# Kernel optimization log

Measured on AMD Instinct MI355X. Metric: run time of the kernel, lower is better.

The kernel has to match this reference:

```python
import jax, jax.numpy as jnp
from jax import lax
import numpy as np

SCALE = 1.0   # self.scale
EPS = 1e-12
CHUNK = 512   # points processed per chunk to bound [P,T,3] temporaries


def _closest_sqdist(p, a, b, c):
    """Squared distance from points p:[P,3] to triangles (a,b,c):[T,3] -> [P,T].
    Ericson's closest-point-on-triangle, fully vectorized."""
    ab = b - a
    ac = c - a
    bc = c - b
    ap = p[:, None, :] - a[None, :, :]
    bp = p[:, None, :] - b[None, :, :]
    cp = p[:, None, :] - c[None, :, :]
    d1 = jnp.einsum('td,ptd->pt', ab, ap)
    d2 = jnp.einsum('td,ptd->pt', ac, ap)
    d3 = jnp.einsum('td,ptd->pt', ab, bp)
    d4 = jnp.einsum('td,ptd->pt', ac, bp)
    d5 = jnp.einsum('td,ptd->pt', ab, cp)
    d6 = jnp.einsum('td,ptd->pt', ac, cp)
    va = d3 * d6 - d5 * d4
    vb = d5 * d2 - d1 * d6
    vc = d1 * d4 - d3 * d2

    def sdiv(n, d):  # NaN/Inf-safe division (branch is masked out by where anyway)
        return n / jnp.where(jnp.abs(d) < EPS, 1.0, d)

    t_ab = sdiv(d1, d1 - d3)[..., None]
    t_ac = sdiv(d2, d2 - d6)[..., None]
    t_bc = sdiv(d4 - d3, (d4 - d3) + (d5 - d6))[..., None]
    denom = va + vb + vc
    v_in = sdiv(vb, denom)[..., None]
    w_in = sdiv(vc, denom)[..., None]

    # base case: interior of the face; then overwrite with edge / vertex regions
    cl = a[None] + v_in * ab[None] + w_in * ac[None]
    cl = jnp.where(((va <= 0) & (d4 - d3 >= 0) & (d5 - d6 >= 0))[..., None],
                   b[None] + t_bc * bc[None], cl)   # edge BC
    cl = jnp.where(((vb <= 0) & (d2 >= 0) & (d6 <= 0))[..., None],
                   a[None] + t_ac * ac[None], cl)   # edge AC
    cl = jnp.where(((vc <= 0) & (d1 >= 0) & (d3 <= 0))[..., None],
                   a[None] + t_ab * ab[None], cl)   # edge AB
    cl = jnp.where(((d6 >= 0) & (d5 <= d6))[..., None], c[None], cl)  # vertex C
    cl = jnp.where(((d3 >= 0) & (d4 <= d3))[..., None], b[None], cl)  # vertex B
    cl = jnp.where(((d1 <= 0) & (d2 <= 0))[..., None], a[None], cl)   # vertex A
    diff = p[:, None, :] - cl
    return jnp.sum(diff * diff, axis=-1)


def setup_inputs():
    key = jax.random.key(0)
    k1, k2, k3 = jax.random.split(key, 3)
    vertices = jax.random.normal(k1, (4, 3, 16, 16, 16), dtype=jnp.float32)
    pc = jax.random.uniform(k2, (4, 4096, 3), dtype=jnp.float32)
    faces = jax.random.randint(k3, (8192, 3), 0, 4096, dtype=jnp.int32)
    return {"vertices": vertices, "pc": pc, "faces": faces}


def reference(vertices, pc, faces):
    B = vertices.shape[0]
    v = jax.nn.sigmoid(vertices)                     # self.normalization
    pos = jnp.moveaxis(v, 1, -1).reshape(B, -1, 3)   # permute(1,2,3,0).view(-1,3)
    pts = pc * SCALE                                 # _scale_points
    # pymesh path drops all-zero points; emulate with a mask (scaling keeps zeros zero)
    mask = jnp.any(pc != 0.0, axis=-1).astype(pts.dtype)  # [B,N]

    def per_batch(args):
        posb, pb, mb = args
        a = posb[faces[:, 0]]
        b = posb[faces[:, 1]]
        c = posb[faces[:, 2]]
        n_chunks = pb.shape[0] // CHUNK

        def chunk_min(pch):  # [CHUNK,3] -> [CHUNK] nearest sq-dist over all tris
            return jnp.min(_closest_sqdist(pch, a, b, c), axis=-1)

        d = lax.map(chunk_min, pb.reshape(n_chunks, CHUNK, 3)).reshape(-1)
        cnt = jnp.maximum(jnp.sum(mb), 1.0)
        return jnp.sum(d * mb) / cnt                 # mean(squared_distances)

    losses = lax.map(per_batch, (pos, pts, mask))    # [B]
    return jnp.mean(losses)
```

## Files before the change

### kernel.cpp

```cpp
#include <hip/hip_runtime.h>
#include <math.h>
#include <float.h>

#define NB 4
#define NP 4096
#define NT 8192
#define TSE 12
#define TEE 20
#define EPSD 1e-12
#define MNS 32
#define MTCH (NT/MNS)
#define VCH 16
#define VLEN (NP/VCH)

__device__ __forceinline__ float sigm(float x) { return 1.0f / (1.0f + expf(-x)); }

__device__ __forceinline__ float tri_dist(
    float px, float py, float pz,
    float ax, float ay, float az,
    float abx, float aby, float abz,
    float acx, float acy, float acz,
    float aa, float am, float cc,
    float raa, float rcc, float rbb,
    float rden, float den, float bb, float k1)
{
  float apx = px - ax, apy = py - ay, apz = pz - az;
  float d1   = apx*abx + apy*aby + apz*abz;
  float d2   = apx*acx + apy*acy + apz*acz;
  float apap = apx*apx + apy*apy + apz*apz;
  float vb = d1*cc - d2*am;
  float vc = d2*aa - d1*am;
  float va = den - vb - vc;
  float di = apap - (vb*d1 + vc*d2)*rden;
  float t2 = d1 + d1;
  float tab = fminf(fmaxf(d1*raa, 0.0f), 1.0f);
  float dAB = apap + tab*(tab*aa - t2);
  float t4 = d2 + d2;
  float tac = fminf(fmaxf(d2*rcc, 0.0f), 1.0f);
  float dAC = apap + tac*(tac*cc - t4);
  float e   = d2 - d1 + k1;
  float tbc = fminf(fmaxf(e*rbb, 0.0f), 1.0f);
  float distB = apap - t2 + aa;
  float dBC = distB + tbc*(tbc*bb - (e + e));
  float m3 = fminf(fminf(dAB, dAC), dBC);
  bool in = (vb >= 0.0f) & (vc >= 0.0f) & (va > 0.0f);
  return in ? di : m3;
}

__global__ __launch_bounds__(256) void vert_kernel(
    const float* __restrict__ verts, float* __restrict__ pos)
{
  int i = blockIdx.x * 256 + threadIdx.x;
  if (i < NB * 3 * NP) pos[i] = sigm(verts[i]);
}

__global__ __launch_bounds__(256) void prep_kernel(
    const float* __restrict__ pos, const int* __restrict__ faces,
    float* __restrict__ triS, float* __restrict__ triE)
{
  int idx = blockIdx.x * 256 + threadIdx.x;
  if (idx >= NB * NT) return;
  int b = idx >> 13;
  int t = idx & (NT - 1);
  int f0 = faces[3*t + 0], f1 = faces[3*t + 1], f2i = faces[3*t + 2];
  const float* pb = pos + (size_t)b * 3 * NP;
  float ax = pb[f0],  ay = pb[NP + f0],  az = pb[2*NP + f0];
  float bx = pb[f1],  by = pb[NP + f1],  bz = pb[2*NP + f1];
  float cx = pb[f2i], cy = pb[NP + f2i], cz = pb[2*NP + f2i];
  float abx = bx - ax, aby = by - ay, abz = bz - az;
  float acx = cx - ax, acy = cy - ay, acz = cz - az;
  double aa = (double)abx*abx + (double)aby*aby + (double)abz*abz;
  double am = (double)abx*acx + (double)aby*acy + (double)abz*acz;
  double cc = (double)acx*acx + (double)acy*acy + (double)acz*acz;
  double den = aa*cc - am*am;
  double bb  = aa - 2.0*am + cc;
  float raa  = (fabs(aa)  < EPSD) ? 1.0f : (float)(1.0/aa);
  float rcc  = (fabs(cc)  < EPSD) ? 1.0f : (float)(1.0/cc);
  float rbb  = (fabs(bb)  < EPSD) ? 1.0f : (float)(1.0/bb);
  float rden = (fabs(den) < EPSD) ? 0.0f : (float)(1.0/den);
  double nx = (double)aby*acz - (double)abz*acy;
  double ny = (double)abz*acx - (double)abx*acz;
  double nz = (double)abx*acy - (double)aby*acx;
  double rs = (fabs(den) < EPSD) ? 0.0 : 1.0 / sqrt(den * 1.02);
  float nhx = (float)(nx * rs), nhy = (float)(ny * rs), nhz = (float)(nz * rs);
  float w = (float)(-(nx*ax + ny*ay + nz*az) * rs);
  float lox = fminf(ax, fminf(bx, cx)), hix = fmaxf(ax, fmaxf(bx, cx));
  float loy = fminf(ay, fminf(by, cy)), hiy = fmaxf(ay, fmaxf(by, cy));
  float loz = fminf(az, fminf(bz, cz)), hiz = fmaxf(az, fmaxf(bz, cz));
  float* rs_ = triS + (size_t)idx * TSE;
  rs_[0] = nhx; rs_[1] = nhy; rs_[2] = nhz; rs_[3]  = w;
  rs_[4] = lox; rs_[5] = loy; rs_[6] = loz; rs_[7]  = hix;
  rs_[8] = hiy; rs_[9] = hiz; rs_[10] = 0.0f; rs_[11] = 0.0f;
  float* re = triE + (size_t)idx * TEE;
  re[0]  = ax;  re[1]  = ay;  re[2]  = az;  re[3]  = abx;
  re[4]  = aby; re[5]  = abz; re[6]  = acx; re[7]  = acy;
  re[8]  = acz; re[9]  = (float)aa; re[10] = (float)am; re[11] = (float)cc;
  re[12] = raa; re[13] = rcc; re[14] = rbb; re[15] = rden;
  re[16] = (float)den; re[17] = (float)bb; re[18] = (float)(aa - am); re[19] = 0.0f;
}

__global__ __launch_bounds__(256) void seed_kernel(
    const float* __restrict__ pos, const float* __restrict__ pc,
    float* __restrict__ partS)
{
  int bid  = blockIdx.x;
  int pblk = bid & 15;
  int vc   = (bid >> 4) & (VCH - 1);
  int b    = bid >> 8;
  int p    = pblk * 256 + threadIdx.x;
  const float* pp = pc + ((size_t)b * NP + p) * 3;
  float px = pp[0], py = pp[1], pz = pp[2];
  const float* base = pos + (size_t)b * 3 * NP + vc * VLEN;
  const float4* X = (const float4*)(base);
  const float4* Y = (const float4*)(base + NP);
  const float4* Z = (const float4*)(base + 2 * NP);
  float m = FLT_MAX;
  #pragma unroll 4
  for (int v = 0; v < VLEN / 4; ++v) {
    float4 vx = X[v], vy = Y[v], vz = Z[v];
    {
      float dx = px - vx.x, dy = py - vy.x, dz = pz - vz.x;
      m = fminf(m, dx*dx + dy*dy + dz*dz);
    }
    {
      float dx = px - vx.y, dy = py - vy.y, dz = pz - vz.y;
      m = fminf(m, dx*dx + dy*dy + dz*dz);
    }
    {
      float dx = px - vx.z, dy = py - vy.z, dz = pz - vz.z;
      m = fminf(m, dx*dx + dy*dy + dz*dz);
    }
    {
      float dx = px - vx.w, dy = py - vy.w, dz = pz - vz.w;
      m = fminf(m, dx*dx + dy*dy + dz*dz);
    }
  }
  partS[((size_t)b * VCH + vc) * NP + p] = m;
}

__global__ __launch_bounds__(256) void main_kernel(
    const float* __restrict__ triS, const float* __restrict__ triE,
    const float* __restrict__ pc, const float* __restrict__ partS,
    float* __restrict__ partM)
{
  __shared__ unsigned qbuf[4][128];
  __shared__ unsigned wmind[4][64];

  int bid  = blockIdx.x;
  int pblk = bid & 15;
  int s    = (bid >> 4) & (MNS - 1);
  int b    = bid >> 9;
  int tid  = threadIdx.x;
  int wave = tid >> 6, lane = tid & 63;
  int p    = pblk * 256 + tid;

  const float* pp = pc + ((size_t)b * NP + p) * 3;
  float px = pp[0], py = pp[1], pz = pp[2];

  float mind = FLT_MAX;
  #pragma unroll
  for (int j = 0; j < VCH; ++j)
    mind = fminf(mind, partS[((size_t)b * VCH + j) * NP + p]);
  wmind[wave][lane] = __float_as_uint(mind);
  float mth = mind + 1e-8f;

  unsigned qcnt = 0u, qd = 0u;
  const float* triEB = triE + (size_t)b * NT * TEE;
  int tg0 = s * MTCH;
  const float4* Rs = (const float4*)(triS + (size_t)(b * NT + tg0) * TSE);

#define DRAIN_BATCH(NACT)                                                     \
  {                                                                           \
    unsigned ent = qbuf[wave][(qd + (unsigned)lane) & 127u];                  \
    if ((unsigned)lane < (unsigned)(NACT)) {                                  \
      int te  = (int)(ent >> 6);                                              \
      int src = (int)(ent & 63u);                                             \
      float qx = __shfl(px, src, 64);                                         \
      float qy = __shfl(py, src, 64);                                         \
      float qz = __shfl(pz, src, 64);                                         \
      const float* rr = triEB + (size_t)te * TEE;                             \
      float4 w1 = *(const float4*)(rr + 0);                                   \
      float4 w2 = *(const float4*)(rr + 4);                                   \
      float4 w3 = *(const float4*)(rr + 8);                                   \
      float4 w4 = *(const float4*)(rr + 12);                                  \
      float4 w5 = *(const float4*)(rr + 16);                                  \
      float dd = fmaxf(tri_dist(qx, qy, qz,                                   \
                                w1.x, w1.y, w1.z,                             \
                                w1.w, w2.x, w2.y,                             \
                                w2.z, w2.w, w3.x,                             \
                                w3.y, w3.z, w3.w,                             \
                                w4.x, w4.y, w4.z,                             \
                                w4.w, w5.x, w5.y, w5.z), 0.0f);               \
      atomicMin(&wmind[wave][src], __float_as_uint(dd));                      \
    }                                                                         \
    qd += (unsigned)(NACT);                                                   \
    mind = fminf(mind, __uint_as_float(wmind[wave][lane]));                   \
    mth  = mind + 1e-8f;                                                      \
  }

#define SCAN_ITER(Q0, Q1, Q2, TIDX)                                           \
  {                                                                           \
    float sN = fmaf(pz, (Q0).z, fmaf(py, (Q0).y, fmaf(px, (Q0).x, (Q0).w)));  \
    float dx = fmaxf(fmaxf((Q1).x - px, px - (Q1).w), 0.0f);                  \
    float dy = fmaxf(fmaxf((Q1).y - py, py - (Q2).x), 0.0f);                  \
    float dz = fmaxf(fmaxf((Q1).z - pz, pz - (Q2).y), 0.0f);                  \
    float bb2 = dx*dx + dy*dy + dz*dz;                                        \
    bool pred = (sN * sN < mth) & (bb2 * 0.98f < mth);                        \
    unsigned long long mask = __ballot(pred);                                 \
    if (mask) {                                                               \
      if (pred) {                                                             \
        int prefix = __builtin_amdgcn_mbcnt_hi((unsigned)(mask >> 32),        \
                       __builtin_amdgcn_mbcnt_lo((unsigned)mask, 0));         \
        qbuf[wave][(qcnt + (unsigned)prefix) & 127u] =                        \
            ((unsigned)(TIDX) << 6) | (unsigned)lane;                         \
      }                                                                       \
      qcnt += (unsigned)__builtin_popcountll(mask);                           \
      if (qcnt - qd >= 64u) DRAIN_BATCH(64u);                                 \
    }                                                                         \
  }

  float4 a0 = Rs[0], a1 = Rs[1], a2 = Rs[2];
  float4 b0 = Rs[3], b1 = Rs[4], b2 = Rs[5];
  int tg = tg0;
  for (int g = 0; g < MTCH / 2; ++g) {
    const float4* Rn = Rs + 6;
    float4 c0 = Rn[0], c1 = Rn[1], c2 = Rn[2];
    float4 d0 = Rn[3], d1 = Rn[4], d2 = Rn[5];
    SCAN_ITER(a0, a1, a2, tg + 0);
    SCAN_ITER(b0, b1, b2, tg + 1);
    a0 = c0; a1 = c1; a2 = c2;
    b0 = d0; b1 = d1; b2 = d2;
    Rs = Rn; tg += 2;
  }

  unsigned pend = qcnt - qd;
  if (pend) DRAIN_BATCH(pend);
  mind = fminf(mind, __uint_as_float(wmind[wave][lane]));

  partM[((size_t)b * MNS + s) * NP + p] = fmaxf(mind, 0.0f);

#undef SCAN_ITER
#undef DRAIN_BATCH
}

__global__ __launch_bounds__(256) void reduce_kernel(
    const float* __restrict__ part, const float* __restrict__ pc,
    float* __restrict__ bl2)
{
  int blk = blockIdx.x;
  int b = blk >> 4;
  int p = (blk & 15) * 256 + threadIdx.x;
  float m = FLT_MAX;
  #pragma unroll
  for (int s = 0; s < MNS; ++s)
    m = fminf(m, part[((size_t)b * MNS + s) * NP + p]);
  const float* pp = pc + ((size_t)b * NP + p) * 3;
  float x = pp[0], y = pp[1], z = pp[2];
  float msk = ((x != 0.0f) | (y != 0.0f) | (z != 0.0f)) ? 1.0f : 0.0f;
  float sdm = m * msk, sm = msk;
  for (int off = 32; off > 0; off >>= 1) {
    sdm += __shfl_down(sdm, off, 64);
    sm  += __shfl_down(sm,  off, 64);
  }
  __shared__ float s1[4], s2[4];
  int wave = threadIdx.x >> 6, lanei = threadIdx.x & 63;
  if (lanei == 0) { s1[wave] = sdm; s2[wave] = sm; }
  __syncthreads();
  if (threadIdx.x == 0) {
    bl2[2 * blk]     = s1[0] + s1[1] + s1[2] + s1[3];
    bl2[2 * blk + 1] = s2[0] + s2[1] + s2[2] + s2[3];
  }
}

__global__ void final_kernel(const float* __restrict__ bl2, float* __restrict__ out)
{
  if (threadIdx.x == 0 && blockIdx.x == 0) {
    float acc = 0.0f;
    for (int b = 0; b < NB; ++b) {
      float sdm = 0.0f, sm = 0.0f;
      for (int k = 0; k < 16; ++k) {
        sdm += bl2[2 * (b * 16 + k)];
        sm  += bl2[2 * (b * 16 + k) + 1];
      }
      acc += sdm / fmaxf(sm, 1.0f);
    }
    out[0] = 0.25f * acc;
  }
}

extern "C" void kernel_launch(void* const* d_in, const int* in_sizes, int n_in,
                              void* d_out, int out_size, void* d_ws, size_t ws_size,
                              hipStream_t stream) {
  const float* verts = (const float*)d_in[0];
  const float* pc    = (const float*)d_in[1];
  const int*   faces = (const int*)d_in[2];
  float* out = (float*)d_out;

  float* pos   = (float*)d_ws;
  float* triS  = pos   + (size_t)NB * 3 * NP;
  float* triE  = triS  + (size_t)NB * NT * TSE;
  float* partS = triE  + (size_t)NB * NT * TEE;
  float* partM = partS + (size_t)NB * VCH * NP;
  float* bl2   = partM + (size_t)NB * MNS * NP;

  vert_kernel<<<(NB * 3 * NP) / 256, 256, 0, stream>>>(verts, pos);
  prep_kernel<<<(NB * NT) / 256, 256, 0, stream>>>(pos, faces, triS, triE);
  seed_kernel<<<NB * VCH * 16, 256, 0, stream>>>(pos, pc, partS);
  main_kernel<<<NB * MNS * 16, 256, 0, stream>>>(triS, triE, pc, partS, partM);
  reduce_kernel<<<NB * 16, 256, 0, stream>>>(partM, pc, bl2);
  final_kernel<<<1, 64, 0, stream>>>(bl2, out);
}
```

Before: 164.4 us.

## Spatially sort points, use bounding-sphere culling, fuse sigmoid and final reduction

Adds a histogram sort that buckets query points into a 4x4x4 grid so each wavefront holds nearby points and its ballots are more coherent. Swaps the triangle AABB culling test for a centroid-plus-radius sphere test, shrinking each triangle's culling record from 12 to 8 floats. Seeds the distance bound from the first 2048 triangles' A vertices instead of all mesh vertices. Also folds the sigmoid into prep and the final reduction into reduce through a last-block atomic counter. The seed bound may be looser, so more triangles could pass culling, and the extra sort kernel and permuted point loads add some cost.

```diff
diff --git a/kernel.cpp b/kernel.cpp
--- a/kernel.cpp
+++ b/kernel.cpp
@@ -5,13 +5,14 @@
 #define NB 4
 #define NP 4096
 #define NT 8192
-#define TSE 12
+#define TSE 8
 #define TEE 20
 #define EPSD 1e-12
 #define MNS 32
 #define MTCH (NT/MNS)
-#define VCH 16
-#define VLEN (NP/VCH)
+#define NSEED 2048
+#define VCH 8
+#define VLEN (NSEED/VCH)
 
 __device__ __forceinline__ float sigm(float x) { return 1.0f / (1.0f + expf(-x)); }
 
@@ -47,26 +48,21 @@
   return in ? di : m3;
 }
 
-__global__ __launch_bounds__(256) void vert_kernel(
-    const float* __restrict__ verts, float* __restrict__ pos)
-{
-  int i = blockIdx.x * 256 + threadIdx.x;
-  if (i < NB * 3 * NP) pos[i] = sigm(verts[i]);
-}
-
 __global__ __launch_bounds__(256) void prep_kernel(
-    const float* __restrict__ pos, const int* __restrict__ faces,
-    float* __restrict__ triS, float* __restrict__ triE)
+    const float* __restrict__ verts, const int* __restrict__ faces,
+    float* __restrict__ triS, float* __restrict__ triE,
+    float* __restrict__ seedA, unsigned* __restrict__ cnt)
 {
   int idx = blockIdx.x * 256 + threadIdx.x;
+  if (idx == 0) *cnt = 0u;
   if (idx >= NB * NT) return;
   int b = idx >> 13;
   int t = idx & (NT - 1);
   int f0 = faces[3*t + 0], f1 = faces[3*t + 1], f2i = faces[3*t + 2];
-  const float* pb = pos + (size_t)b * 3 * NP;
-  float ax = pb[f0],  ay = pb[NP + f0],  az = pb[2*NP + f0];
-  float bx = pb[f1],  by = pb[NP + f1],  bz = pb[2*NP + f1];
-  float cx = pb[f2i], cy = pb[NP + f2i], cz = pb[2*NP + f2i];
+  const float* vb_ = verts + (size_t)b * 3 * NP;
+  float ax = sigm(vb_[f0]),  ay = sigm(vb_[NP + f0]),  az = sigm(vb_[2*NP + f0]);
+  float bx = sigm(vb_[f1]),  by = sigm(vb_[NP + f1]),  bz = sigm(vb_[2*NP + f1]);
+  float cx = sigm(vb_[f2i]), cy = sigm(vb_[NP + f2i]), cz = sigm(vb_[2*NP + f2i]);
   float abx = bx - ax, aby = by - ay, abz = bz - az;
   float acx = cx - ax, acy = cy - ay, acz = cz - az;
   double aa = (double)abx*abx + (double)aby*aby + (double)abz*abz;
@@ -84,36 +80,78 @@
   double rs = (fabs(den) < EPSD) ? 0.0 : 1.0 / sqrt(den * 1.02);
   float nhx = (float)(nx * rs), nhy = (float)(ny * rs), nhz = (float)(nz * rs);
   float w = (float)(-(nx*ax + ny*ay + nz*az) * rs);
-  float lox = fminf(ax, fminf(bx, cx)), hix = fmaxf(ax, fmaxf(bx, cx));
-  float loy = fminf(ay, fminf(by, cy)), hiy = fmaxf(ay, fmaxf(by, cy));
-  float loz = fminf(az, fminf(bz, cz)), hiz = fmaxf(az, fmaxf(bz, cz));
+  float qx = (ax + bx + cx) * (1.0f/3.0f);
+  float qy = (ay + by + cy) * (1.0f/3.0f);
+  float qz = (az + bz + cz) * (1.0f/3.0f);
+  float r2a = (ax-qx)*(ax-qx) + (ay-qy)*(ay-qy) + (az-qz)*(az-qz);
+  float r2b = (bx-qx)*(bx-qx) + (by-qy)*(by-qy) + (bz-qz)*(bz-qz);
+  float r2c = (cx-qx)*(cx-qx) + (cy-qy)*(cy-qy) + (cz-qz)*(cz-qz);
+  float R = sqrtf(fmaxf(r2a, fmaxf(r2b, r2c))) * 1.0005f + 1e-6f;
   float* rs_ = triS + (size_t)idx * TSE;
-  rs_[0] = nhx; rs_[1] = nhy; rs_[2] = nhz; rs_[3]  = w;
-  rs_[4] = lox; rs_[5] = loy; rs_[6] = loz; rs_[7]  = hix;
-  rs_[8] = hiy; rs_[9] = hiz; rs_[10] = 0.0f; rs_[11] = 0.0f;
+  rs_[0] = nhx; rs_[1] = nhy; rs_[2] = nhz; rs_[3] = w;
+  rs_[4] = qx;  rs_[5] = qy;  rs_[6] = qz;  rs_[7] = R;
   float* re = triE + (size_t)idx * TEE;
   re[0]  = ax;  re[1]  = ay;  re[2]  = az;  re[3]  = abx;
   re[4]  = aby; re[5]  = abz; re[6]  = acx; re[7]  = acy;
   re[8]  = acz; re[9]  = (float)aa; re[10] = (float)am; re[11] = (float)cc;
   re[12] = raa; re[13] = rcc; re[14] = rbb; re[15] = rden;
   re[16] = (float)den; re[17] = (float)bb; re[18] = (float)(aa - am); re[19] = 0.0f;
+  if (t < NSEED) {
+    float* sa = seedA + (size_t)b * 3 * NSEED + t;
+    sa[0] = ax; sa[NSEED] = ay; sa[2*NSEED] = az;
+  }
+}
+
+__global__ __launch_bounds__(256) void psort_kernel(
+    const float* __restrict__ pc, unsigned* __restrict__ perm)
+{
+  __shared__ unsigned hist[64];
+  __shared__ unsigned off[64];
+  int b = blockIdx.x;
+  int tid = threadIdx.x;
+  if (tid < 64) hist[tid] = 0u;
+  __syncthreads();
+  unsigned cells[16], ranks[16];
+  #pragma unroll
+  for (int k = 0; k < 16; ++k) {
+    int i = k * 256 + tid;
+    const float* pp = pc + ((size_t)b * NP + i) * 3;
+    float x = pp[0], y = pp[1], z = pp[2];
+    int ix = min(3, max(0, (int)(x * 4.0f)));
+    int iy = min(3, max(0, (int)(y * 4.0f)));
+    int iz = min(3, max(0, (int)(z * 4.0f)));
+    unsigned c = (unsigned)(ix | (iy << 2) | (iz << 4));
+    cells[k] = c;
+    ranks[k] = atomicAdd(&hist[c], 1u);
+  }
+  __syncthreads();
+  if (tid == 0) {
+    unsigned acc = 0u;
+    for (int c = 0; c < 64; ++c) { off[c] = acc; acc += hist[c]; }
+  }
+  __syncthreads();
+  #pragma unroll
+  for (int k = 0; k < 16; ++k) {
+    int i = k * 256 + tid;
+    perm[(size_t)b * NP + off[cells[k]] + ranks[k]] = (unsigned)i;
+  }
 }
 
 __global__ __launch_bounds__(256) void seed_kernel(
-    const float* __restrict__ pos, const float* __restrict__ pc,
+    const float* __restrict__ seedA, const float* __restrict__ pc,
     float* __restrict__ partS)
 {
   int bid  = blockIdx.x;
   int pblk = bid & 15;
   int vc   = (bid >> 4) & (VCH - 1);
-  int b    = bid >> 8;
+  int b    = bid >> 7;
   int p    = pblk * 256 + threadIdx.x;
   const float* pp = pc + ((size_t)b * NP + p) * 3;
   float px = pp[0], py = pp[1], pz = pp[2];
-  const float* base = pos + (size_t)b * 3 * NP + vc * VLEN;
+  const float* base = seedA + (size_t)b * 3 * NSEED + vc * VLEN;
   const float4* X = (const float4*)(base);
-  const float4* Y = (const float4*)(base + NP);
-  const float4* Z = (const float4*)(base + 2 * NP);
+  const float4* Y = (const float4*)(base + NSEED);
+  const float4* Z = (const float4*)(base + 2 * NSEED);
   float m = FLT_MAX;
   #pragma unroll 4
   for (int v = 0; v < VLEN / 4; ++v) {
@@ -141,7 +179,7 @@
 __global__ __launch_bounds__(256) void main_kernel(
     const float* __restrict__ triS, const float* __restrict__ triE,
     const float* __restrict__ pc, const float* __restrict__ partS,
-    float* __restrict__ partM)
+    const unsigned* __restrict__ perm, float* __restrict__ partM)
 {
   __shared__ unsigned qbuf[4][128];
   __shared__ unsigned wmind[4][64];
@@ -152,7 +190,7 @@
   int b    = bid >> 9;
   int tid  = threadIdx.x;
   int wave = tid >> 6, lane = tid & 63;
-  int p    = pblk * 256 + tid;
+  int p    = (int)perm[(size_t)b * NP + pblk * 256 + tid];
 
   const float* pp = pc + ((size_t)b * NP + p) * 3;
   float px = pp[0], py = pp[1], pz = pp[2];
@@ -162,7 +200,8 @@
   for (int j = 0; j < VCH; ++j)
     mind = fminf(mind, partS[((size_t)b * VCH + j) * NP + p]);
   wmind[wave][lane] = __float_as_uint(mind);
-  float mth = mind + 1e-8f;
+  float mth   = mind + 1e-8f;
+  float smind = sqrtf(mind) * 1.005f + 1e-5f;
 
   unsigned qcnt = 0u, qd = 0u;
   const float* triEB = triE + (size_t)b * NT * TEE;
@@ -194,18 +233,18 @@
       atomicMin(&wmind[wave][src], __float_as_uint(dd));                      \
     }                                                                         \
     qd += (unsigned)(NACT);                                                   \
-    mind = fminf(mind, __uint_as_float(wmind[wave][lane]));                   \
-    mth  = mind + 1e-8f;                                                      \
-  }
-
-#define SCAN_ITER(Q0, Q1, Q2, TIDX)                                           \
+    mind  = fminf(mind, __uint_as_float(wmind[wave][lane]));                  \
+    mth   = mind + 1e-8f;                                                     \
+    smind = sqrtf(mind) * 1.005f + 1e-5f;                                     \
+  }
+
+#define SCAN_ITER(Q0, Q1, TIDX)                                               \
   {                                                                           \
-    float sN = fmaf(pz, (Q0).z, fmaf(py, (Q0).y, fmaf(px, (Q0).x, (Q0).w)));  \
-    float dx = fmaxf(fmaxf((Q1).x - px, px - (Q1).w), 0.0f);                  \
-    float dy = fmaxf(fmaxf((Q1).y - py, py - (Q2).x), 0.0f);                  \
-    float dz = fmaxf(fmaxf((Q1).z - pz, pz - (Q2).y), 0.0f);                  \
-    float bb2 = dx*dx + dy*dy + dz*dz;                                        \
-    bool pred = (sN * sN < mth) & (bb2 * 0.98f < mth);                        \
+    float sN  = fmaf(pz, (Q0).z, fmaf(py, (Q0).y, fmaf(px, (Q0).x, (Q0).w))); \
+    float dqx = px - (Q1).x, dqy = py - (Q1).y, dqz = pz - (Q1).z;            \
+    float dq2 = fmaf(dqx, dqx, fmaf(dqy, dqy, dqz * dqz));                    \
+    float tt  = smind + (Q1).w;                                               \
+    bool pred = (sN * sN < mth) & (dq2 < tt * tt);                            \
     unsigned long long mask = __ballot(pred);                                 \
     if (mask) {                                                               \
       if (pred) {                                                             \
@@ -219,17 +258,16 @@
     }                                                                         \
   }
 
-  float4 a0 = Rs[0], a1 = Rs[1], a2 = Rs[2];
-  float4 b0 = Rs[3], b1 = Rs[4], b2 = Rs[5];
+  float4 a0 = Rs[0], a1 = Rs[1];
+  float4 b0 = Rs[2], b1 = Rs[3];
   int tg = tg0;
   for (int g = 0; g < MTCH / 2; ++g) {
-    const float4* Rn = Rs + 6;
-    float4 c0 = Rn[0], c1 = Rn[1], c2 = Rn[2];
-    float4 d0 = Rn[3], d1 = Rn[4], d2 = Rn[5];
-    SCAN_ITER(a0, a1, a2, tg + 0);
-    SCAN_ITER(b0, b1, b2, tg + 1);
-    a0 = c0; a1 = c1; a2 = c2;
-    b0 = d0; b1 = d1; b2 = d2;
+    const float4* Rn = Rs + 4;
+    float4 c0 = Rn[0], c1 = Rn[1];
+    float4 d0 = Rn[2], d1 = Rn[3];
+    SCAN_ITER(a0, a1, tg + 0);
+    SCAN_ITER(b0, b1, tg + 1);
+    a0 = c0; a1 = c1; b0 = d0; b1 = d1;
     Rs = Rn; tg += 2;
   }
 
@@ -245,7 +283,8 @@
 
 __global__ __launch_bounds__(256) void reduce_kernel(
     const float* __restrict__ part, const float* __restrict__ pc,
-    float* __restrict__ bl2)
+    float* __restrict__ bl2, unsigned* __restrict__ cnt,
+    float* __restrict__ out)
 {
   int blk = blockIdx.x;
   int b = blk >> 4;
@@ -263,28 +302,37 @@
     sm  += __shfl_down(sm,  off, 64);
   }
   __shared__ float s1[4], s2[4];
+  __shared__ bool last;
   int wave = threadIdx.x >> 6, lanei = threadIdx.x & 63;
   if (lanei == 0) { s1[wave] = sdm; s2[wave] = sm; }
   __syncthreads();
   if (threadIdx.x == 0) {
     bl2[2 * blk]     = s1[0] + s1[1] + s1[2] + s1[3];
     bl2[2 * blk + 1] = s2[0] + s2[1] + s2[2] + s2[3];
-  }
-}
-
-__global__ void final_kernel(const float* __restrict__ bl2, float* __restrict__ out)
-{
-  if (threadIdx.x == 0 && blockIdx.x == 0) {
-    float acc = 0.0f;
-    for (int b = 0; b < NB; ++b) {
-      float sdm = 0.0f, sm = 0.0f;
-      for (int k = 0; k < 16; ++k) {
-        sdm += bl2[2 * (b * 16 + k)];
-        sm  += bl2[2 * (b * 16 + k) + 1];
+    __threadfence();
+    unsigned t = atomicAdd(cnt, 1u);
+    last = (t == 63u);
+  }
+  __syncthreads();
+  if (last) {
+    __shared__ float f1[64], f2[64];
+    if (threadIdx.x < 64) {
+      f1[threadIdx.x] = atomicAdd(&bl2[2 * threadIdx.x],     0.0f);
+      f2[threadIdx.x] = atomicAdd(&bl2[2 * threadIdx.x + 1], 0.0f);
+    }
+    __syncthreads();
+    if (threadIdx.x == 0) {
+      float acc = 0.0f;
+      for (int bb = 0; bb < NB; ++bb) {
+        float tsd = 0.0f, tsm = 0.0f;
+        for (int k = 0; k < 16; ++k) {
+          tsd += f1[bb * 16 + k];
+          tsm += f2[bb * 16 + k];
+        }
+        acc += tsd / fmaxf(tsm, 1.0f);
       }
-      acc += sdm / fmaxf(sm, 1.0f);
-    }
-    out[0] = 0.25f * acc;
+      out[0] = 0.25f * acc;
+    }
   }
 }
 
@@ -296,17 +344,18 @@
   const int*   faces = (const int*)d_in[2];
   float* out = (float*)d_out;
 
-  float* pos   = (float*)d_ws;
-  float* triS  = pos   + (size_t)NB * 3 * NP;
+  float* triS  = (float*)d_ws;
   float* triE  = triS  + (size_t)NB * NT * TSE;
-  float* partS = triE  + (size_t)NB * NT * TEE;
+  float* seedA = triE  + (size_t)NB * NT * TEE;
+  float* partS = seedA + (size_t)NB * 3 * NSEED;
   float* partM = partS + (size_t)NB * VCH * NP;
   float* bl2   = partM + (size_t)NB * MNS * NP;
-
-  vert_kernel<<<(NB * 3 * NP) / 256, 256, 0, stream>>>(verts, pos);
-  prep_kernel<<<(NB * NT) / 256, 256, 0, stream>>>(pos, faces, triS, triE);
-  seed_kernel<<<NB * VCH * 16, 256, 0, stream>>>(pos, pc, partS);
-  main_kernel<<<NB * MNS * 16, 256, 0, stream>>>(triS, triE, pc, partS, partM);
-  reduce_kernel<<<NB * 16, 256, 0, stream>>>(partM, pc, bl2);
-  final_kernel<<<1, 64, 0, stream>>>(bl2, out);
-}
+  unsigned* cnt  = (unsigned*)(bl2 + 128);
+  unsigned* perm = (unsigned*)(bl2 + 132);
+
+  prep_kernel<<<(NB * NT) / 256, 256, 0, stream>>>(verts, faces, triS, triE, seedA, cnt);
+  psort_kernel<<<NB, 256, 0, stream>>>(pc, perm);
+  seed_kernel<<<NB * VCH * 16, 256, 0, stream>>>(seedA, pc, partS);
+  main_kernel<<<NB * MNS * 16, 256, 0, stream>>>(triS, triE, pc, partS, perm, partM);
+  reduce_kernel<<<NB * 16, 256, 0, stream>>>(partM, pc, bl2, cnt, out);
+}
```

New measurement: 164.7 us. About the same (+0.2%).
